# Performance work log

Hardware: AMD Instinct MI355X
Metric: run time of the kernel (lower is better)

Reference implementation:

```python
import jax, jax.numpy as jnp
import numpy as np

HIDDEN = 128
N_LAYERS = 6
N_NODES = 50000
N_EDGES = 640000


def _glorot(key, shape):
    fan_in, fan_out = shape[0], shape[1]
    lim = (6.0 / (fan_in + fan_out)) ** 0.5
    return jax.random.uniform(key, shape, jnp.float32, -lim, lim)


def setup_inputs() -> dict:
    key = jax.random.key(0)
    ks = jax.random.split(key, 8)
    pos = jax.random.normal(ks[0], (N_NODES, 3), jnp.float32)
    edge_attr = jax.random.normal(ks[1], (N_EDGES, 3), jnp.float32)
    edge_index = jax.random.randint(ks[2], (2, N_EDGES), 0, N_NODES, jnp.int64)
    enc_w = _glorot(ks[3], (3, HIDDEN)); enc_b = jnp.zeros((HIDDEN,), jnp.float32)
    dec_w = _glorot(ks[4], (HIDDEN, 3)); dec_b = jnp.zeros((3,), jnp.float32)
    lk = jax.random.split(ks[5], 4 * N_LAYERS)
    edge_w1 = jnp.stack([_glorot(lk[4 * i + 0], (3 * HIDDEN, HIDDEN)) for i in range(N_LAYERS)])
    edge_w2 = jnp.stack([_glorot(lk[4 * i + 1], (HIDDEN, HIDDEN)) for i in range(N_LAYERS)])
    node_w1 = jnp.stack([_glorot(lk[4 * i + 2], (2 * HIDDEN, HIDDEN)) for i in range(N_LAYERS)])
    node_w2 = jnp.stack([_glorot(lk[4 * i + 3], (HIDDEN, HIDDEN)) for i in range(N_LAYERS)])
    edge_b1 = jnp.zeros((N_LAYERS, HIDDEN), jnp.float32)
    edge_b2 = jnp.zeros((N_LAYERS, HIDDEN), jnp.float32)
    node_b1 = jnp.zeros((N_LAYERS, HIDDEN), jnp.float32)
    node_b2 = jnp.zeros((N_LAYERS, HIDDEN), jnp.float32)
    return dict(pos=pos, edge_attr=edge_attr, edge_index=edge_index,
                enc_w=enc_w, enc_b=enc_b, dec_w=dec_w, dec_b=dec_b,
                edge_w1=edge_w1, edge_b1=edge_b1, edge_w2=edge_w2, edge_b2=edge_b2,
                node_w1=node_w1, node_b1=node_b1, node_w2=node_w2, node_b2=node_b2)


def _interaction(x, ef, src, dst, ew1, eb1, ew2, eb2, nw1, nb1, nw2, nb2, n_nodes):
    # message: concat(x_i=x[dst], x_j=x[src], edge_feature) -> edge MLP
    m = jnp.concatenate([x[dst], x[src], ef], axis=-1)            # [E, 3H]
    m = jax.nn.relu(m @ ew1 + eb1) @ ew2 + eb2                     # [E, H]
    # scatter-mean by target node
    sums = jax.ops.segment_sum(m, dst, num_segments=n_nodes)      # [N, H]
    cnt = jax.ops.segment_sum(jnp.ones((m.shape[0],), m.dtype), dst, num_segments=n_nodes)
    aggr = sums / jnp.maximum(cnt, 1.0)[:, None]
    node = jnp.concatenate([x, aggr], axis=-1)                     # [N, 2H]
    node = jax.nn.relu(node @ nw1 + nb1) @ nw2 + nb2               # [N, H]
    return x + node, ef + m


def reference(pos, edge_attr, edge_index, enc_w, enc_b, dec_w, dec_b,
              edge_w1, edge_b1, edge_w2, edge_b2,
              node_w1, node_b1, node_w2, node_b2):
    n_nodes = pos.shape[0]
    src = edge_index[0]
    dst = edge_index[1]
    x = jnp.zeros((n_nodes, HIDDEN), jnp.float32)
    ef = edge_attr @ enc_w + enc_b
    for i in range(N_LAYERS):
        x, ef = _interaction(x, ef, src, dst,
                             edge_w1[i], edge_b1[i], edge_w2[i], edge_b2[i],
                             node_w1[i], node_b1[i], node_w2[i], node_b2[i], n_nodes)
    out = x @ dec_w + dec_b                                        # [N, 3]
    # F.normalize(dim=1, eps=1e-12)
    norm = jnp.linalg.norm(out, axis=1, keepdims=True)
    return out / jnp.maximum(norm, 1e-12)
```

## Files before the change

kernel.cpp:

```cpp
#include <hip/hip_runtime.h>
#include <cstdint>

#define HIDDEN  128
#define NLAYERS 6
#define NNODES  50000
#define NEDGES  640000

typedef short short8 __attribute__((ext_vector_type(8)));
typedef float f32x4  __attribute__((ext_vector_type(4)));

__device__ __forceinline__ float bf2f(unsigned short u) {
    return __uint_as_float(((unsigned int)u) << 16);
}
__device__ __forceinline__ unsigned short f2bf(float f) {
    unsigned int u = __float_as_uint(f);
    unsigned int r = u + 0x7FFFu + ((u >> 16) & 1u);
    return (unsigned short)(r >> 16);
}
__device__ __forceinline__ unsigned int pack2(float a, float b) {
    return (unsigned int)f2bf(a) | ((unsigned int)f2bf(b) << 16);
}
__device__ __forceinline__ void unpack8(uint4 v, float* f) {
    f[0] = bf2f((unsigned short)(v.x & 0xffff)); f[1] = bf2f((unsigned short)(v.x >> 16));
    f[2] = bf2f((unsigned short)(v.y & 0xffff)); f[3] = bf2f((unsigned short)(v.y >> 16));
    f[4] = bf2f((unsigned short)(v.z & 0xffff)); f[5] = bf2f((unsigned short)(v.z >> 16));
    f[6] = bf2f((unsigned short)(v.w & 0xffff)); f[7] = bf2f((unsigned short)(v.w >> 16));
}

__global__ void detect_kernel(const int* __restrict__ ei, int* __restrict__ flag)
{
    int lane = threadIdx.x;
    int v = ei[2 * lane + 1];
    unsigned long long b = __ballot(v != 0);
    if (lane == 0) *flag = (b != 0ULL) ? 1 : 0;
}

__global__ void normidx_kernel(const int* __restrict__ ei, const int* __restrict__ flag,
                               int* __restrict__ s32, int* __restrict__ d32)
{
    int e = blockIdx.x * blockDim.x + threadIdx.x;
    if (e >= NEDGES) return;
    int s, d;
    if (*flag) { s = ei[e]; d = ei[NEDGES + e]; }
    else       { s = ei[2 * e]; d = ei[2 * (NEDGES + e)]; }
    s32[e] = min(max(s, 0), NNODES - 1);
    d32[e] = min(max(d, 0), NNODES - 1);
}

__global__ void degree_kernel(const int* __restrict__ dst, int* __restrict__ deg)
{
    int e = blockIdx.x * blockDim.x + threadIdx.x;
    if (e < NEDGES) atomicAdd(&deg[dst[e]], 1);
}

#define SCAN_T 1024
__global__ void scan_kernel(const int* __restrict__ deg, int* __restrict__ off,
                            int* __restrict__ cursor)
{
    __shared__ int part[SCAN_T];
    const int t = threadIdx.x;
    const int CH = (NNODES + SCAN_T - 1) / SCAN_T;
    const int base = t * CH;
    int s = 0;
    for (int i = 0; i < CH; ++i) {
        int idx = base + i;
        if (idx < NNODES) s += deg[idx];
    }
    part[t] = s;
    __syncthreads();
    for (int d = 1; d < SCAN_T; d <<= 1) {
        int v = (t >= d) ? part[t - d] : 0;
        __syncthreads();
        part[t] += v;
        __syncthreads();
    }
    int run = (t == 0) ? 0 : part[t - 1];
    for (int i = 0; i < CH; ++i) {
        int idx = base + i;
        if (idx < NNODES) {
            off[idx] = run;
            cursor[idx] = run;
            run += deg[idx];
        }
    }
    if (t == SCAN_T - 1) off[NNODES] = run;
}

__global__ void scatter_kernel(const int* __restrict__ s32, const int* __restrict__ d32,
                               int* __restrict__ cursor,
                               int* __restrict__ sp, int* __restrict__ dp, int* __restrict__ ep)
{
    int e = blockIdx.x * blockDim.x + threadIdx.x;
    if (e >= NEDGES) return;
    int d = d32[e];
    int p = atomicAdd(&cursor[d], 1);
    sp[p] = s32[e];
    dp[p] = d;
    ep[p] = e;
}

__global__ void transpose_kernel(const float* __restrict__ W, unsigned short* __restrict__ WT,
                                 int K, int N, int L)
{
    long idx = (long)blockIdx.x * 256 + threadIdx.x;
    long tot = (long)L * K * N;
    if (idx >= tot) return;
    int kn = (int)(idx % ((long)K * N));
    int l  = (int)(idx / ((long)K * N));
    int k = kn / N;
    int n = kn % N;
    WT[(long)l * K * N + (long)n * K + k] = f2bf(W[idx]);
}

__global__ void encode_kernel(const float* __restrict__ ea,
                              const float* __restrict__ w,
                              const float* __restrict__ b,
                              const int* __restrict__ ep,
                              unsigned short* __restrict__ ef)
{
    int idx = blockIdx.x * blockDim.x + threadIdx.x;
    int p = idx >> 5;
    if (p >= NEDGES) return;
    int e = ep[p];
    int j = (idx & 31) << 2;
    float a0 = ea[e * 3 + 0], a1 = ea[e * 3 + 1], a2 = ea[e * 3 + 2];
    float4 w0 = *(const float4*)(w + 0 * HIDDEN + j);
    float4 w1 = *(const float4*)(w + 1 * HIDDEN + j);
    float4 w2 = *(const float4*)(w + 2 * HIDDEN + j);
    float4 bb = *(const float4*)(b + j);
    ushort4 o;
    o.x = f2bf(fmaf(a0, w0.x, fmaf(a1, w1.x, fmaf(a2, w2.x, bb.x))));
    o.y = f2bf(fmaf(a0, w0.y, fmaf(a1, w1.y, fmaf(a2, w2.y, bb.y))));
    o.z = f2bf(fmaf(a0, w0.z, fmaf(a1, w1.z, fmaf(a2, w2.z, bb.z))));
    o.w = f2bf(fmaf(a0, w0.w, fmaf(a1, w1.w, fmaf(a2, w2.w, bb.w))));
    *(ushort4*)(ef + (long)p * HIDDEN + j) = o;
}

__global__ __launch_bounds__(256, 3)
void edge_layer_mfma(const unsigned short* __restrict__ Xa,
                     const unsigned short* __restrict__ Xb,
                     unsigned short* __restrict__ ef,
                     float* __restrict__ sums,
                     const int* __restrict__ sp,
                     const int* __restrict__ dp,
                     const unsigned short* __restrict__ W1T,
                     const float* __restrict__ b1,
                     const unsigned short* __restrict__ W2T,
                     const float* __restrict__ b2)
{
    __shared__ __align__(16) unsigned char buf[45056];
    unsigned short* As = (unsigned short*)buf;
    unsigned short* Hs = (unsigned short*)buf;
    unsigned short* Bs = (unsigned short*)(buf + 34816);
    __shared__ int dv[128];
    __shared__ int sv[128];

    const int tid = threadIdx.x;
    const long eb = (long)blockIdx.x * 128;
    if (tid < 128) dv[tid]       = dp[eb + tid];
    else           sv[tid - 128] = sp[eb + tid - 128];

    const int lane = tid & 63;
    const int wv   = tid >> 6;
    const int mn   = lane & 15;
    const int q    = lane >> 4;
    const int rr   = tid >> 1;
    const int o    = (tid & 1) << 4;
    const int bn   = tid >> 1;
    const int bk   = (tid & 1) << 4;

    f32x4 acc[2][8];
#pragma unroll
    for (int h = 0; h < 2; ++h)
#pragma unroll
        for (int t = 0; t < 8; ++t) acc[h][t] = (f32x4)0.0f;

    short8 efold0[4], efold1[4];

    uint4 pa0, pa1, pw0, pw1;
    {
        const unsigned short* epp = ef + (eb + rr) * HIDDEN + o;
        pa0 = *(const uint4*)epp;
        pa1 = *(const uint4*)(epp + 8);
        const unsigned short* wp = W1T + (long)bn * 384 + 256 + bk;
        pw0 = *(const uint4*)wp;
        pw1 = *(const uint4*)(wp + 8);
    }

    for (int c = 0; c < 4; ++c) {
        *(uint4*)&As[rr * 40 + o]      = pa0;
        *(uint4*)&As[rr * 40 + o + 8]  = pa1;
        *(uint4*)&Bs[bn * 40 + bk]     = pw0;
        *(uint4*)&Bs[bn * 40 + bk + 8] = pw1;
        __syncthreads();

        if (c + 1 < 4) {
            const int cn = c + 1;
            const unsigned short* epp = ef + (eb + rr) * HIDDEN + (cn << 5) + o;
            pa0 = *(const uint4*)epp;
            pa1 = *(const uint4*)(epp + 8);
            const unsigned short* wp = W1T + (long)bn * 384 + 256 + (cn << 5) + bk;
            pw0 = *(const uint4*)wp;
            pw1 = *(const uint4*)(wp + 8);
        }

        short8 af0 = *(short8*)&As[(wv * 32 + mn) * 40 + (q << 3)];
        short8 af1 = *(short8*)&As[(wv * 32 + 16 + mn) * 40 + (q << 3)];
        efold0[c] = af0;
        efold1[c] = af1;
#pragma unroll
        for (int nt = 0; nt < 8; ++nt) {
            short8 bf = *(short8*)&Bs[(nt * 16 + mn) * 40 + (q << 3)];
            acc[0][nt] = __builtin_amdgcn_mfma_f32_16x16x32_bf16(af0, bf, acc[0][nt], 0, 0, 0);
            acc[1][nt] = __builtin_amdgcn_mfma_f32_16x16x32_bf16(af1, bf, acc[1][nt], 0, 0, 0);
        }
        __syncthreads();
    }

#pragma unroll
    for (int h = 0; h < 2; ++h)
#pragma unroll
        for (int nt = 0; nt < 8; ++nt)
#pragma unroll
            for (int r = 0; r < 4; ++r)
                Hs[(wv * 32 + h * 16 + q * 4 + r) * 136 + nt * 16 + mn] = f2bf(acc[h][nt][r]);

    {
        const int row  = wv * 32 + (lane >> 1);
        const int ch   = (lane & 1) << 6;
        const unsigned short* xap = Xa + (long)dv[row] * HIDDEN + ch;
        const unsigned short* xbp = Xb + (long)sv[row] * HIDDEN + ch;
        unsigned short* hp = &Hs[row * 136 + ch];
#pragma unroll
        for (int i = 0; i < 8; ++i) {
            uint4 va = *(const uint4*)(xap + (i << 3));
            uint4 vb = *(const uint4*)(xbp + (i << 3));
            uint4 vp = *(uint4*)(hp + (i << 3));
            float fa[8], fb[8], fp[8];
            unpack8(va, fa); unpack8(vb, fb); unpack8(vp, fp);
            const float* bp = b1 + ch + (i << 3);
            uint4 nw;
            float h0 = fmaxf(fp[0] + fa[0] + fb[0] + bp[0], 0.0f);
            float h1 = fmaxf(fp[1] + fa[1] + fb[1] + bp[1], 0.0f);
            float h2 = fmaxf(fp[2] + fa[2] + fb[2] + bp[2], 0.0f);
            float h3 = fmaxf(fp[3] + fa[3] + fb[3] + bp[3], 0.0f);
            float h4 = fmaxf(fp[4] + fa[4] + fb[4] + bp[4], 0.0f);
            float h5 = fmaxf(fp[5] + fa[5] + fb[5] + bp[5], 0.0f);
            float h6 = fmaxf(fp[6] + fa[6] + fb[6] + bp[6], 0.0f);
            float h7 = fmaxf(fp[7] + fa[7] + fb[7] + bp[7], 0.0f);
            nw.x = pack2(h0, h1); nw.y = pack2(h2, h3);
            nw.z = pack2(h4, h5); nw.w = pack2(h6, h7);
            *(uint4*)(hp + (i << 3)) = nw;
        }
    }

    f32x4 acc2[2][8];
#pragma unroll
    for (int h = 0; h < 2; ++h)
#pragma unroll
        for (int t = 0; t < 8; ++t) acc2[h][t] = (f32x4)0.0f;
    {
        const unsigned short* wp = W2T + (long)bn * 128 + bk;
        pw0 = *(const uint4*)wp;
        pw1 = *(const uint4*)(wp + 8);
    }
    for (int c = 0; c < 4; ++c) {
        *(uint4*)&Bs[bn * 40 + bk]     = pw0;
        *(uint4*)&Bs[bn * 40 + bk + 8] = pw1;
        __syncthreads();
        if (c + 1 < 4) {
            const unsigned short* wp = W2T + (long)bn * 128 + ((c + 1) << 5) + bk;
            pw0 = *(const uint4*)wp;
            pw1 = *(const uint4*)(wp + 8);
        }
        short8 af0 = *(short8*)&Hs[(wv * 32 + mn) * 136 + (c << 5) + (q << 3)];
        short8 af1 = *(short8*)&Hs[(wv * 32 + 16 + mn) * 136 + (c << 5) + (q << 3)];
#pragma unroll
        for (int nt = 0; nt < 8; ++nt) {
            short8 bf = *(short8*)&Bs[(nt * 16 + mn) * 40 + (q << 3)];
            acc2[0][nt] = __builtin_amdgcn_mfma_f32_16x16x32_bf16(af0, bf, acc2[0][nt], 0, 0, 0);
            acc2[1][nt] = __builtin_amdgcn_mfma_f32_16x16x32_bf16(af1, bf, acc2[1][nt], 0, 0, 0);
        }
        __syncthreads();
    }

#pragma unroll
    for (int h = 0; h < 2; ++h)
#pragma unroll
        for (int nt = 0; nt < 8; ++nt) {
            float b2v = b2[nt * 16 + mn];
#pragma unroll
            for (int r = 0; r < 4; ++r)
                Hs[(wv * 32 + h * 16 + q * 4 + r) * 136 + nt * 16 + mn] = f2bf(acc2[h][nt][r] + b2v);
        }

#pragma unroll
    for (int h = 0; h < 2; ++h) {
        const int row = wv * 32 + h * 16 + mn;
        unsigned short* ep_ = ef + (eb + row) * HIDDEN + (q << 3);
#pragma unroll
        for (int c = 0; c < 4; ++c) {
            uint4 mh = *(uint4*)&Hs[row * 136 + (c << 5) + (q << 3)];
            float m[8], e[8];
            unpack8(mh, m);
            short8 eo = h ? efold1[c] : efold0[c];
            uint4 eu = *(uint4*)&eo;
            unpack8(eu, e);
            uint4 nw;
            nw.x = pack2(e[0] + m[0], e[1] + m[1]);
            nw.y = pack2(e[2] + m[2], e[3] + m[3]);
            nw.z = pack2(e[4] + m[4], e[5] + m[5]);
            nw.w = pack2(e[6] + m[6], e[7] + m[7]);
            *(uint4*)(ep_ + (c << 5)) = nw;
        }
    }

    {
        const int cp = (tid & 63) << 1;
        const int qr = tid >> 6;
        float s0 = 0.0f, s1 = 0.0f;
        int cur = dv[qr * 32];
        for (int r = 0; r < 32; ++r) {
            const int row = qr * 32 + r;
            const int d = dv[row];
            if (d != cur) {
                atomicAdd(&sums[(long)cur * HIDDEN + cp], s0);
                atomicAdd(&sums[(long)cur * HIDDEN + cp + 1], s1);
                s0 = 0.0f; s1 = 0.0f;
                cur = d;
            }
            unsigned int u = *(unsigned int*)&Hs[row * 136 + cp];
            s0 += bf2f((unsigned short)(u & 0xffff));
            s1 += bf2f((unsigned short)(u >> 16));
        }
        atomicAdd(&sums[(long)cur * HIDDEN + cp], s0);
        atomicAdd(&sums[(long)cur * HIDDEN + cp + 1], s1);
    }
}

__global__ __launch_bounds__(256, 4)
void node_layer_mfma(float* __restrict__ x,
                     float* __restrict__ sums,
                     const int* __restrict__ deg,
                     const unsigned short* __restrict__ N1T,
                     const float* __restrict__ b1,
                     const unsigned short* __restrict__ N2T,
                     const float* __restrict__ b2,
                     const unsigned short* __restrict__ W1Tn,
                     unsigned short* __restrict__ Xa,
                     unsigned short* __restrict__ Xb)
{
    __shared__ __align__(16) unsigned short As[64 * 40];
    __shared__ __align__(16) unsigned short Bs[128 * 40];
    __shared__ __align__(16) unsigned short Hs[64 * 136];
    __shared__ float cInv[64];

    const int tid = threadIdx.x;
    const long n0 = (long)blockIdx.x * 64;
    if (tid < 64) {
        long n = n0 + tid;
        cInv[tid] = (n < NNODES) ? 1.0f / fmaxf((float)deg[n], 1.0f) : 0.0f;
    }

    const int lane = tid & 63;
    const int wv   = tid >> 6;
    const int mn   = lane & 15;
    const int q    = lane >> 4;
    const int srow = tid >> 2;
    const int sseg = tid & 3;
    const int bn   = tid >> 1;
    const int bk   = (tid & 1) << 4;

    long nr = n0 + srow;
    if (nr >= NNODES) nr = NNODES - 1;

    __syncthreads();

    f32x4 acc[8];
#pragma unroll
    for (int t = 0; t < 8; ++t) acc[t] = (f32x4)0.0f;

    float4 pa0, pa1;
    uint4 pb0, pb1;
    {
        const float* spx = x + nr * HIDDEN + (sseg << 3);
        pa0 = *(const float4*)spx;
        pa1 = *(const float4*)(spx + 4);
        const unsigned short* wp = N1T + (long)bn * 256 + bk;
        pb0 = *(const uint4*)wp;
        pb1 = *(const uint4*)(wp + 8);
    }
    float scCur = 1.0f;
    for (int c = 0; c < 8; ++c) {
        {
            uint4 w;
            w.x = pack2(pa0.x * scCur, pa0.y * scCur); w.y = pack2(pa0.z * scCur, pa0.w * scCur);
            w.z = pack2(pa1.x * scCur, pa1.y * scCur); w.w = pack2(pa1.z * scCur, pa1.w * scCur);
            *(uint4*)&As[srow * 40 + (sseg << 3)] = w;
        }
        *(uint4*)&Bs[bn * 40 + bk]     = pb0;
        *(uint4*)&Bs[bn * 40 + bk + 8] = pb1;
        __syncthreads();
        if (c + 1 < 8) {
            const int cn = c + 1;
            const float* base = (cn < 4) ? x : sums;
            scCur = (cn < 4) ? 1.0f : cInv[srow];
            const float* spx = base + nr * HIDDEN + ((cn & 3) << 5) + (sseg << 3);
            pa0 = *(const float4*)spx;
            pa1 = *(const float4*)(spx + 4);
            const unsigned short* wp = N1T + (long)bn * 256 + (cn << 5) + bk;
            pb0 = *(const uint4*)wp;
            pb1 = *(const uint4*)(wp + 8);
        }
        short8 af = *(short8*)&As[(wv * 16 + mn) * 40 + (q << 3)];
#pragma unroll
        for (int nt = 0; nt < 8; ++nt) {
            short8 bf = *(short8*)&Bs[(nt * 16 + mn) * 40 + (q << 3)];
            acc[nt] = __builtin_amdgcn_mfma_f32_16x16x32_bf16(af, bf, acc[nt], 0, 0, 0);
        }
        __syncthreads();
    }

    {
        long row = n0 + srow;
        if (row < NNODES) {
            float4 z = make_float4(0.f, 0.f, 0.f, 0.f);
            float* p = sums + row * HIDDEN + (sseg << 5);
#pragma unroll
            for (int i = 0; i < 8; ++i) ((float4*)p)[i] = z;
        }
    }

#pragma unroll
    for (int nt = 0; nt < 8; ++nt) {
        float b1v = b1[nt * 16 + mn];
#pragma unroll
        for (int r = 0; r < 4; ++r) {
            float hv = fmaxf(acc[nt][r] + b1v, 0.0f);
            Hs[(wv * 16 + q * 4 + r) * 136 + nt * 16 + mn] = f2bf(hv);
        }
    }

    f32x4 acc2[8];
#pragma unroll
    for (int t = 0; t < 8; ++t) acc2[t] = (f32x4)0.0f;
    {
        const unsigned short* wp = N2T + (long)bn * 128 + bk;
        pb0 = *(const uint4*)wp;
        pb1 = *(const uint4*)(wp + 8);
    }
    for (int c = 0; c < 4; ++c) {
        *(uint4*)&Bs[bn * 40 + bk]     = pb0;
        *(uint4*)&Bs[bn * 40 + bk + 8] = pb1;
        __syncthreads();
        if (c + 1 < 4) {
            const unsigned short* wp = N2T + (long)bn * 128 + ((c + 1) << 5) + bk;
            pb0 = *(const uint4*)wp;
            pb1 = *(const uint4*)(wp + 8);
        }
        short8 af = *(short8*)&Hs[(wv * 16 + mn) * 136 + (c << 5) + (q << 3)];
#pragma unroll
        for (int nt = 0; nt < 8; ++nt) {
            short8 bf = *(short8*)&Bs[(nt * 16 + mn) * 40 + (q << 3)];
            acc2[nt] = __builtin_amdgcn_mfma_f32_16x16x32_bf16(af, bf, acc2[nt], 0, 0, 0);
        }
        __syncthreads();
    }

#pragma unroll
    for (int nt = 0; nt < 8; ++nt) {
        float b2v = b2[nt * 16 + mn];
#pragma unroll
        for (int r = 0; r < 4; ++r) {
            long row = n0 + wv * 16 + q * 4 + r;
            float xn = 0.0f;
            if (row < NNODES) {
                float* p = x + row * HIDDEN + nt * 16 + mn;
                xn = *p + acc2[nt][r] + b2v;
                *p = xn;
            }
            Hs[(wv * 16 + q * 4 + r) * 136 + nt * 16 + mn] = f2bf(xn);
        }
    }

    if (W1Tn) {
#pragma unroll
        for (int half = 0; half < 2; ++half) {
            f32x4 accN[8];
#pragma unroll
            for (int t = 0; t < 8; ++t) accN[t] = (f32x4)0.0f;
            const int kbase = half << 7;
            {
                const unsigned short* wp = W1Tn + (long)bn * 384 + kbase + bk;
                pb0 = *(const uint4*)wp;
                pb1 = *(const uint4*)(wp + 8);
            }
            for (int c = 0; c < 4; ++c) {
                *(uint4*)&Bs[bn * 40 + bk]     = pb0;
                *(uint4*)&Bs[bn * 40 + bk + 8] = pb1;
                __syncthreads();
                if (c + 1 < 4) {
                    const unsigned short* wp = W1Tn + (long)bn * 384 + kbase + ((c + 1) << 5) + bk;
                    pb0 = *(const uint4*)wp;
                    pb1 = *(const uint4*)(wp + 8);
                }
                short8 af = *(short8*)&Hs[(wv * 16 + mn) * 136 + (c << 5) + (q << 3)];
#pragma unroll
                for (int nt = 0; nt < 8; ++nt) {
                    short8 bf = *(short8*)&Bs[(nt * 16 + mn) * 40 + (q << 3)];
                    accN[nt] = __builtin_amdgcn_mfma_f32_16x16x32_bf16(af, bf, accN[nt], 0, 0, 0);
                }
                __syncthreads();
            }
            unsigned short* Xout = half ? Xb : Xa;
#pragma unroll
            for (int nt = 0; nt < 8; ++nt) {
#pragma unroll
                for (int r = 0; r < 4; ++r) {
                    long row = n0 + wv * 16 + q * 4 + r;
                    if (row < NNODES) {
                        Xout[row * HIDDEN + nt * 16 + mn] = f2bf(accN[nt][r]);
                    }
                }
            }
        }
    }
}

__global__ void decode_kernel(const float* __restrict__ x,
                              const float* __restrict__ w,
                              const float* __restrict__ b,
                              float* __restrict__ out)
{
    int gid = blockIdx.x * blockDim.x + threadIdx.x;
    int node = gid >> 6;
    int lane = threadIdx.x & 63;
    if (node >= NNODES) return;
    float a0 = 0.f, a1 = 0.f, a2 = 0.f;
#pragma unroll
    for (int k = lane; k < HIDDEN; k += 64) {
        float xv = x[(long)node * HIDDEN + k];
        a0 = fmaf(xv, w[k * 3 + 0], a0);
        a1 = fmaf(xv, w[k * 3 + 1], a1);
        a2 = fmaf(xv, w[k * 3 + 2], a2);
    }
#pragma unroll
    for (int off = 32; off > 0; off >>= 1) {
        a0 += __shfl_down(a0, off);
        a1 += __shfl_down(a1, off);
        a2 += __shfl_down(a2, off);
    }
    if (lane == 0) {
        a0 += b[0]; a1 += b[1]; a2 += b[2];
        float nrm = sqrtf(a0 * a0 + a1 * a1 + a2 * a2);
        float inv = 1.0f / fmaxf(nrm, 1e-12f);
        out[(long)node * 3 + 0] = a0 * inv;
        out[(long)node * 3 + 1] = a1 * inv;
        out[(long)node * 3 + 2] = a2 * inv;
    }
}

extern "C" void kernel_launch(void* const* d_in, const int* in_sizes, int n_in,
                              void* d_out, int out_size, void* d_ws, size_t ws_size,
                              hipStream_t stream)
{
    const float* edge_attr = (const float*)d_in[1];
    const int*   ei        = (const int*)d_in[2];
    const float* enc_w     = (const float*)d_in[3];
    const float* enc_b     = (const float*)d_in[4];
    const float* dec_w     = (const float*)d_in[5];
    const float* dec_b     = (const float*)d_in[6];
    const float* edge_w1   = (const float*)d_in[7];
    const float* edge_b1   = (const float*)d_in[8];
    const float* edge_w2   = (const float*)d_in[9];
    const float* edge_b2   = (const float*)d_in[10];
    const float* node_w1   = (const float*)d_in[11];
    const float* node_b1   = (const float*)d_in[12];
    const float* node_w2   = (const float*)d_in[13];
    const float* node_b2   = (const float*)d_in[14];

    char* ws = (char*)d_ws;
    unsigned short* ef  = (unsigned short*)(ws);
    float* x      = (float*)(ws + 163840000L);
    float* sums   = (float*)(ws + 189440000L);
    int*   src32  = (int*)  (ws + 215040000L);
    int*   dst32  = (int*)  (ws + 217600000L);
    int*   sp     = (int*)  (ws + 220160000L);
    int*   dp     = (int*)  (ws + 222720000L);
    int*   eperm  = (int*)  (ws + 225280000L);
    int*   deg    = (int*)  (ws + 227840000L);
    int*   off    = (int*)  (ws + 228040704L);
    int*   cursor = (int*)  (ws + 228241408L);
    int*   flag   = (int*)  (ws + 228442112L);
    unsigned short* W1T = (unsigned short*)(ws + 228442176L);
    unsigned short* W2T = (unsigned short*)(ws + 229032000L);
    unsigned short* N1T = (unsigned short*)(ws + 229228608L);
    unsigned short* N2T = (unsigned short*)(ws + 229621824L);
    unsigned short* Xa  = (unsigned short*)(ws + 229818432L);
    unsigned short* Xb  = (unsigned short*)(ws + 242618432L);

    float* out = (float*)d_out;

    hipMemsetAsync(x, 0, (size_t)NNODES * HIDDEN * sizeof(float), stream);
    hipMemsetAsync(sums, 0, (size_t)NNODES * HIDDEN * sizeof(float), stream);
    hipMemsetAsync(deg, 0, 200704, stream);
    hipMemsetAsync(Xa, 0, 25600000, stream);

    detect_kernel<<<1, 64, 0, stream>>>(ei, flag);
    normidx_kernel<<<(NEDGES + 255) / 256, 256, 0, stream>>>(ei, flag, src32, dst32);
    degree_kernel<<<(NEDGES + 255) / 256, 256, 0, stream>>>(dst32, deg);
    scan_kernel<<<1, SCAN_T, 0, stream>>>(deg, off, cursor);
    scatter_kernel<<<(NEDGES + 255) / 256, 256, 0, stream>>>(src32, dst32, cursor, sp, dp, eperm);
    encode_kernel<<<(NEDGES * 32 + 255) / 256, 256, 0, stream>>>(edge_attr, enc_w, enc_b, eperm, ef);

    transpose_kernel<<<(6 * 384 * 128 + 255) / 256, 256, 0, stream>>>(edge_w1, W1T, 384, 128, 6);
    transpose_kernel<<<(6 * 128 * 128 + 255) / 256, 256, 0, stream>>>(edge_w2, W2T, 128, 128, 6);
    transpose_kernel<<<(6 * 256 * 128 + 255) / 256, 256, 0, stream>>>(node_w1, N1T, 256, 128, 6);
    transpose_kernel<<<(6 * 128 * 128 + 255) / 256, 256, 0, stream>>>(node_w2, N2T, 128, 128, 6);

    for (int l = 0; l < NLAYERS; ++l) {
        edge_layer_mfma<<<NEDGES / 128, 256, 0, stream>>>(
            Xa, Xb, ef, sums, sp, dp,
            W1T + (long)l * 384 * 128, edge_b1 + (long)l * HIDDEN,
            W2T + (long)l * 128 * 128, edge_b2 + (long)l * HIDDEN);
        const unsigned short* w1next = (l + 1 < NLAYERS) ? (W1T + (long)(l + 1) * 384 * 128) : nullptr;
        node_layer_mfma<<<(NNODES + 63) / 64, 256, 0, stream>>>(
            x, sums, deg,
            N1T + (long)l * 256 * 128, node_b1 + (long)l * HIDDEN,
            N2T + (long)l * 128 * 128, node_b2 + (long)l * HIDDEN,
            w1next, Xa, Xb);
    }

    decode_kernel<<<(NNODES * 64 + 255) / 256, 256, 0, stream>>>(x, dec_w, dec_b, out);
}
```

Before: 1.544 ms.

## Pre-swizzle node MLP weights into MFMA fragment order and drop LDS staging

Adds a swizzle kernel that reorders node and next-layer edge weights into the per-lane MFMA B-fragment layout, so the node kernel reads B operands straight from global/L2 instead of staging them through shared memory with barriers. The node kernel now uses 32-row, 128-thread blocks, loads the whole x/aggr row into LDS once, and zeroes sums up front. This removes many __syncthreads and LDS round trips, at the cost of every wave re-reading weights from cache and smaller blocks.

```diff
diff --git a/kernel.cpp b/kernel.cpp
--- a/kernel.cpp
+++ b/kernel.cpp
@@ -110,6 +110,23 @@
     int k = kn / N;
     int n = kn % N;
     WT[(long)l * K * N + (long)n * K + k] = f2bf(W[idx]);
+}
+
+__global__ void swizzle_kernel(const float* __restrict__ W, unsigned short* __restrict__ out,
+                               int k0, int Ktot, int Ksw, int L)
+{
+    long per = (long)Ksw * 128;
+    long idx = (long)blockIdx.x * 256 + threadIdx.x;
+    if (idx >= (long)L * per) return;
+    int l = (int)(idx / per);
+    int o = (int)(idx % per);
+    int j    = o & 7;
+    int lane = (o >> 3) & 63;
+    int frag = o >> 9;
+    int c = frag >> 3, nt = frag & 7;
+    int k = k0 + c * 32 + (lane >> 4) * 8 + j;
+    int n = nt * 16 + (lane & 15);
+    out[idx] = f2bf(W[(long)l * Ktot * 128 + (long)k * 128 + n]);
 }
 
 __global__ void encode_kernel(const float* __restrict__ ea,
@@ -338,96 +355,68 @@
     }
 }
 
-__global__ __launch_bounds__(256, 4)
+__global__ __launch_bounds__(128, 4)
 void node_layer_mfma(float* __restrict__ x,
                      float* __restrict__ sums,
                      const int* __restrict__ deg,
-                     const unsigned short* __restrict__ N1T,
+                     const unsigned short* __restrict__ N1S,
                      const float* __restrict__ b1,
-                     const unsigned short* __restrict__ N2T,
+                     const unsigned short* __restrict__ N2S,
                      const float* __restrict__ b2,
-                     const unsigned short* __restrict__ W1Tn,
+                     const unsigned short* __restrict__ W1An,
+                     const unsigned short* __restrict__ W1Bn,
                      unsigned short* __restrict__ Xa,
                      unsigned short* __restrict__ Xb)
 {
-    __shared__ __align__(16) unsigned short As[64 * 40];
-    __shared__ __align__(16) unsigned short Bs[128 * 40];
-    __shared__ __align__(16) unsigned short Hs[64 * 136];
-    __shared__ float cInv[64];
-
-    const int tid = threadIdx.x;
-    const long n0 = (long)blockIdx.x * 64;
-    if (tid < 64) {
-        long n = n0 + tid;
-        cInv[tid] = (n < NNODES) ? 1.0f / fmaxf((float)deg[n], 1.0f) : 0.0f;
-    }
-
+    __shared__ __align__(16) unsigned short As[32 * 264];
+    __shared__ __align__(16) unsigned short Hs[32 * 136];
+
+    const int tid  = threadIdx.x;
+    const long n0  = (long)blockIdx.x * 32;
     const int lane = tid & 63;
     const int wv   = tid >> 6;
     const int mn   = lane & 15;
     const int q    = lane >> 4;
-    const int srow = tid >> 2;
-    const int sseg = tid & 3;
-    const int bn   = tid >> 1;
-    const int bk   = (tid & 1) << 4;
-
-    long nr = n0 + srow;
-    if (nr >= NNODES) nr = NNODES - 1;
-
-    __syncthreads();
+
+    {
+        const int row = tid >> 2;
+        const int qt  = (tid & 3) << 5;
+        long nr = n0 + row; if (nr >= NNODES) nr = NNODES - 1;
+        const float ci = 1.0f / fmaxf((float)deg[nr], 1.0f);
+        const float* xr = x + nr * HIDDEN + qt;
+        const float* sr = sums + nr * HIDDEN + qt;
+#pragma unroll
+        for (int i = 0; i < 4; ++i) {
+            float4 v0 = *(const float4*)(xr + i * 8);
+            float4 v1 = *(const float4*)(xr + i * 8 + 4);
+            uint4 u;
+            u.x = pack2(v0.x, v0.y); u.y = pack2(v0.z, v0.w);
+            u.z = pack2(v1.x, v1.y); u.w = pack2(v1.z, v1.w);
+            *(uint4*)&As[row * 264 + qt + i * 8] = u;
+            float4 w0 = *(const float4*)(sr + i * 8);
+            float4 w1 = *(const float4*)(sr + i * 8 + 4);
+            u.x = pack2(w0.x * ci, w0.y * ci); u.y = pack2(w0.z * ci, w0.w * ci);
+            u.z = pack2(w1.x * ci, w1.y * ci); u.w = pack2(w1.z * ci, w1.w * ci);
+            *(uint4*)&As[row * 264 + 128 + qt + i * 8] = u;
+        }
+        if (n0 + row < NNODES) {
+            float4 z = make_float4(0.f, 0.f, 0.f, 0.f);
+            float* p = sums + nr * HIDDEN + qt;
+#pragma unroll
+            for (int i = 0; i < 8; ++i) ((float4*)p)[i] = z;
+        }
+    }
 
     f32x4 acc[8];
 #pragma unroll
     for (int t = 0; t < 8; ++t) acc[t] = (f32x4)0.0f;
-
-    float4 pa0, pa1;
-    uint4 pb0, pb1;
-    {
-        const float* spx = x + nr * HIDDEN + (sseg << 3);
-        pa0 = *(const float4*)spx;
-        pa1 = *(const float4*)(spx + 4);
-        const unsigned short* wp = N1T + (long)bn * 256 + bk;
-        pb0 = *(const uint4*)wp;
-        pb1 = *(const uint4*)(wp + 8);
-    }
-    float scCur = 1.0f;
+#pragma unroll
     for (int c = 0; c < 8; ++c) {
-        {
-            uint4 w;
-            w.x = pack2(pa0.x * scCur, pa0.y * scCur); w.y = pack2(pa0.z * scCur, pa0.w * scCur);
-            w.z = pack2(pa1.x * scCur, pa1.y * scCur); w.w = pack2(pa1.z * scCur, pa1.w * scCur);
-            *(uint4*)&As[srow * 40 + (sseg << 3)] = w;
-        }
-        *(uint4*)&Bs[bn * 40 + bk]     = pb0;
-        *(uint4*)&Bs[bn * 40 + bk + 8] = pb1;
-        __syncthreads();
-        if (c + 1 < 8) {
-            const int cn = c + 1;
-            const float* base = (cn < 4) ? x : sums;
-            scCur = (cn < 4) ? 1.0f : cInv[srow];
-            const float* spx = base + nr * HIDDEN + ((cn & 3) << 5) + (sseg << 3);
-            pa0 = *(const float4*)spx;
-            pa1 = *(const float4*)(spx + 4);
-            const unsigned short* wp = N1T + (long)bn * 256 + (cn << 5) + bk;
-            pb0 = *(const uint4*)wp;
-            pb1 = *(const uint4*)(wp + 8);
-        }
-        short8 af = *(short8*)&As[(wv * 16 + mn) * 40 + (q << 3)];
+        short8 af = *(short8*)&As[(wv * 16 + mn) * 264 + (c << 5) + (q << 3)];
 #pragma unroll
         for (int nt = 0; nt < 8; ++nt) {
-            short8 bf = *(short8*)&Bs[(nt * 16 + mn) * 40 + (q << 3)];
+            short8 bf = *(const short8*)(N1S + (c * 8 + nt) * 512 + lane * 8);
             acc[nt] = __builtin_amdgcn_mfma_f32_16x16x32_bf16(af, bf, acc[nt], 0, 0, 0);
-        }
-        __syncthreads();
-    }
-
-    {
-        long row = n0 + srow;
-        if (row < NNODES) {
-            float4 z = make_float4(0.f, 0.f, 0.f, 0.f);
-            float* p = sums + row * HIDDEN + (sseg << 5);
-#pragma unroll
-            for (int i = 0; i < 8; ++i) ((float4*)p)[i] = z;
         }
     }
 
@@ -444,27 +433,14 @@
     f32x4 acc2[8];
 #pragma unroll
     for (int t = 0; t < 8; ++t) acc2[t] = (f32x4)0.0f;
-    {
-        const unsigned short* wp = N2T + (long)bn * 128 + bk;
-        pb0 = *(const uint4*)wp;
-        pb1 = *(const uint4*)(wp + 8);
-    }
+#pragma unroll
     for (int c = 0; c < 4; ++c) {
-        *(uint4*)&Bs[bn * 40 + bk]     = pb0;
-        *(uint4*)&Bs[bn * 40 + bk + 8] = pb1;
-        __syncthreads();
-        if (c + 1 < 4) {
-            const unsigned short* wp = N2T + (long)bn * 128 + ((c + 1) << 5) + bk;
-            pb0 = *(const uint4*)wp;
-            pb1 = *(const uint4*)(wp + 8);
-        }
         short8 af = *(short8*)&Hs[(wv * 16 + mn) * 136 + (c << 5) + (q << 3)];
 #pragma unroll
         for (int nt = 0; nt < 8; ++nt) {
-            short8 bf = *(short8*)&Bs[(nt * 16 + mn) * 40 + (q << 3)];
+            short8 bf = *(const short8*)(N2S + (c * 8 + nt) * 512 + lane * 8);
             acc2[nt] = __builtin_amdgcn_mfma_f32_16x16x32_bf16(af, bf, acc2[nt], 0, 0, 0);
         }
-        __syncthreads();
     }
 
 #pragma unroll
@@ -483,34 +459,21 @@
         }
     }
 
-    if (W1Tn) {
+    if (W1An) {
 #pragma unroll
         for (int half = 0; half < 2; ++half) {
+            const unsigned short* Bsw = half ? W1Bn : W1An;
             f32x4 accN[8];
 #pragma unroll
             for (int t = 0; t < 8; ++t) accN[t] = (f32x4)0.0f;
-            const int kbase = half << 7;
-            {
-                const unsigned short* wp = W1Tn + (long)bn * 384 + kbase + bk;
-                pb0 = *(const uint4*)wp;
-                pb1 = *(const uint4*)(wp + 8);
-            }
+#pragma unroll
             for (int c = 0; c < 4; ++c) {
-                *(uint4*)&Bs[bn * 40 + bk]     = pb0;
-                *(uint4*)&Bs[bn * 40 + bk + 8] = pb1;
-                __syncthreads();
-                if (c + 1 < 4) {
-                    const unsigned short* wp = W1Tn + (long)bn * 384 + kbase + ((c + 1) << 5) + bk;
-                    pb0 = *(const uint4*)wp;
-                    pb1 = *(const uint4*)(wp + 8);
-                }
                 short8 af = *(short8*)&Hs[(wv * 16 + mn) * 136 + (c << 5) + (q << 3)];
 #pragma unroll
                 for (int nt = 0; nt < 8; ++nt) {
-                    short8 bf = *(short8*)&Bs[(nt * 16 + mn) * 40 + (q << 3)];
+                    short8 bf = *(const short8*)(Bsw + (c * 8 + nt) * 512 + lane * 8);
                     accN[nt] = __builtin_amdgcn_mfma_f32_16x16x32_bf16(af, bf, accN[nt], 0, 0, 0);
                 }
-                __syncthreads();
             }
             unsigned short* Xout = half ? Xb : Xa;
 #pragma unroll
@@ -594,10 +557,12 @@
     int*   flag   = (int*)  (ws + 228442112L);
     unsigned short* W1T = (unsigned short*)(ws + 228442176L);
     unsigned short* W2T = (unsigned short*)(ws + 229032000L);
-    unsigned short* N1T = (unsigned short*)(ws + 229228608L);
-    unsigned short* N2T = (unsigned short*)(ws + 229621824L);
-    unsigned short* Xa  = (unsigned short*)(ws + 229818432L);
-    unsigned short* Xb  = (unsigned short*)(ws + 242618432L);
+    unsigned short* N1S = (unsigned short*)(ws + 229228608L);
+    unsigned short* N2S = (unsigned short*)(ws + 229621824L);
+    unsigned short* W1A = (unsigned short*)(ws + 229818432L);
+    unsigned short* W1B = (unsigned short*)(ws + 230015040L);
+    unsigned short* Xa  = (unsigned short*)(ws + 230211648L);
+    unsigned short* Xb  = (unsigned short*)(ws + 243011648L);
 
     float* out = (float*)d_out;
 
@@ -615,20 +580,23 @@
 
     transpose_kernel<<<(6 * 384 * 128 + 255) / 256, 256, 0, stream>>>(edge_w1, W1T, 384, 128, 6);
     transpose_kernel<<<(6 * 128 * 128 + 255) / 256, 256, 0, stream>>>(edge_w2, W2T, 128, 128, 6);
-    transpose_kernel<<<(6 * 256 * 128 + 255) / 256, 256, 0, stream>>>(node_w1, N1T, 256, 128, 6);
-    transpose_kernel<<<(6 * 128 * 128 + 255) / 256, 256, 0, stream>>>(node_w2, N2T, 128, 128, 6);
+    swizzle_kernel<<<(6 * 256 * 128 + 255) / 256, 256, 0, stream>>>(node_w1, N1S, 0,   256, 256, 6);
+    swizzle_kernel<<<(6 * 128 * 128 + 255) / 256, 256, 0, stream>>>(node_w2, N2S, 0,   128, 128, 6);
+    swizzle_kernel<<<(6 * 128 * 128 + 255) / 256, 256, 0, stream>>>(edge_w1, W1A, 0,   384, 128, 6);
+    swizzle_kernel<<<(6 * 128 * 128 + 255) / 256, 256, 0, stream>>>(edge_w1, W1B, 128, 384, 128, 6);
 
     for (int l = 0; l < NLAYERS; ++l) {
         edge_layer_mfma<<<NEDGES / 128, 256, 0, stream>>>(
             Xa, Xb, ef, sums, sp, dp,
             W1T + (long)l * 384 * 128, edge_b1 + (long)l * HIDDEN,
             W2T + (long)l * 128 * 128, edge_b2 + (long)l * HIDDEN);
-        const unsigned short* w1next = (l + 1 < NLAYERS) ? (W1T + (long)(l + 1) * 384 * 128) : nullptr;
-        node_layer_mfma<<<(NNODES + 63) / 64, 256, 0, stream>>>(
+        const unsigned short* w1an = (l + 1 < NLAYERS) ? (W1A + (long)(l + 1) * 16384) : nullptr;
+        const unsigned short* w1bn = (l + 1 < NLAYERS) ? (W1B + (long)(l + 1) * 16384) : nullptr;
+        node_layer_mfma<<<(NNODES + 31) / 32, 128, 0, stream>>>(
             x, sums, deg,
-            N1T + (long)l * 256 * 128, node_b1 + (long)l * HIDDEN,
-            N2T + (long)l * 128 * 128, node_b2 + (long)l * HIDDEN,
-            w1next, Xa, Xb);
+            N1S + (long)l * 32768, node_b1 + (long)l * HIDDEN,
+            N2S + (long)l * 16384, node_b2 + (long)l * HIDDEN,
+            w1an, w1bn, Xa, Xb);
     }
 
     decode_kernel<<<(NNODES * 64 + 255) / 256, 256, 0, stream>>>(x, dec_w, dec_b, out);
```

New measurement: 1.680 ms. +8.7%, slower.

## Split edge-layer work across 8 waves and alias node-layer shared buffers

Applied to the files above, without the earlier changes.

The edge MLP kernel now runs 512 threads per 128-edge block, so each wave handles 16 rows instead of 32. This halves the accumulator and saved-ef registers per thread and allows more waves in flight to hide gather and atomic latency. The node kernel overlays its A staging buffer with the H buffer in shared memory to lower LDS use and raises its occupancy hint. The cost is that each B fragment read from LDS now feeds half as many MFMAs, and the block barriers cover more waves.

```diff
diff --git a/kernel.cpp b/kernel.cpp
--- a/kernel.cpp
+++ b/kernel.cpp
@@ -136,7 +136,7 @@
     *(ushort4*)(ef + (long)p * HIDDEN + j) = o;
 }
 
-__global__ __launch_bounds__(256, 3)
+__global__ __launch_bounds__(512, 6)
 void edge_layer_mfma(const unsigned short* __restrict__ Xa,
                      const unsigned short* __restrict__ Xb,
                      unsigned short* __restrict__ ef,
@@ -157,82 +157,65 @@
 
     const int tid = threadIdx.x;
     const long eb = (long)blockIdx.x * 128;
-    if (tid < 128) dv[tid]       = dp[eb + tid];
-    else           sv[tid - 128] = sp[eb + tid - 128];
+    if (tid < 128)       dv[tid]       = dp[eb + tid];
+    else if (tid < 256)  sv[tid - 128] = sp[eb + tid - 128];
 
     const int lane = tid & 63;
     const int wv   = tid >> 6;
     const int mn   = lane & 15;
     const int q    = lane >> 4;
-    const int rr   = tid >> 1;
-    const int o    = (tid & 1) << 4;
-    const int bn   = tid >> 1;
-    const int bk   = (tid & 1) << 4;
-
-    f32x4 acc[2][8];
-#pragma unroll
-    for (int h = 0; h < 2; ++h)
-#pragma unroll
-        for (int t = 0; t < 8; ++t) acc[h][t] = (f32x4)0.0f;
-
-    short8 efold0[4], efold1[4];
-
-    uint4 pa0, pa1, pw0, pw1;
-    {
-        const unsigned short* epp = ef + (eb + rr) * HIDDEN + o;
-        pa0 = *(const uint4*)epp;
-        pa1 = *(const uint4*)(epp + 8);
-        const unsigned short* wp = W1T + (long)bn * 384 + 256 + bk;
-        pw0 = *(const uint4*)wp;
-        pw1 = *(const uint4*)(wp + 8);
+    const int rr   = tid >> 2;
+    const int o    = (tid & 3) << 3;
+    const int bn   = tid >> 2;
+    const int bo   = (tid & 3) << 3;
+
+    f32x4 acc[8];
+#pragma unroll
+    for (int t = 0; t < 8; ++t) acc[t] = (f32x4)0.0f;
+
+    short8 efold[4];
+
+    uint4 pa, pw;
+    {
+        pa = *(const uint4*)(ef + (eb + rr) * HIDDEN + o);
+        pw = *(const uint4*)(W1T + (long)bn * 384 + 256 + bo);
     }
 
     for (int c = 0; c < 4; ++c) {
-        *(uint4*)&As[rr * 40 + o]      = pa0;
-        *(uint4*)&As[rr * 40 + o + 8]  = pa1;
-        *(uint4*)&Bs[bn * 40 + bk]     = pw0;
-        *(uint4*)&Bs[bn * 40 + bk + 8] = pw1;
+        *(uint4*)&As[rr * 40 + o]  = pa;
+        *(uint4*)&Bs[bn * 40 + bo] = pw;
         __syncthreads();
 
         if (c + 1 < 4) {
             const int cn = c + 1;
-            const unsigned short* epp = ef + (eb + rr) * HIDDEN + (cn << 5) + o;
-            pa0 = *(const uint4*)epp;
-            pa1 = *(const uint4*)(epp + 8);
-            const unsigned short* wp = W1T + (long)bn * 384 + 256 + (cn << 5) + bk;
-            pw0 = *(const uint4*)wp;
-            pw1 = *(const uint4*)(wp + 8);
-        }
-
-        short8 af0 = *(short8*)&As[(wv * 32 + mn) * 40 + (q << 3)];
-        short8 af1 = *(short8*)&As[(wv * 32 + 16 + mn) * 40 + (q << 3)];
-        efold0[c] = af0;
-        efold1[c] = af1;
+            pa = *(const uint4*)(ef + (eb + rr) * HIDDEN + (cn << 5) + o);
+            pw = *(const uint4*)(W1T + (long)bn * 384 + 256 + (cn << 5) + bo);
+        }
+
+        short8 af = *(short8*)&As[(wv * 16 + mn) * 40 + (q << 3)];
+        efold[c] = af;
 #pragma unroll
         for (int nt = 0; nt < 8; ++nt) {
             short8 bf = *(short8*)&Bs[(nt * 16 + mn) * 40 + (q << 3)];
-            acc[0][nt] = __builtin_amdgcn_mfma_f32_16x16x32_bf16(af0, bf, acc[0][nt], 0, 0, 0);
-            acc[1][nt] = __builtin_amdgcn_mfma_f32_16x16x32_bf16(af1, bf, acc[1][nt], 0, 0, 0);
-        }
-        __syncthreads();
-    }
-
-#pragma unroll
-    for (int h = 0; h < 2; ++h)
-#pragma unroll
-        for (int nt = 0; nt < 8; ++nt)
-#pragma unroll
-            for (int r = 0; r < 4; ++r)
-                Hs[(wv * 32 + h * 16 + q * 4 + r) * 136 + nt * 16 + mn] = f2bf(acc[h][nt][r]);
-
-    {
-        const int row  = wv * 32 + (lane >> 1);
-        const int ch   = (lane & 1) << 6;
+            acc[nt] = __builtin_amdgcn_mfma_f32_16x16x32_bf16(af, bf, acc[nt], 0, 0, 0);
+        }
+        __syncthreads();
+    }
+
+#pragma unroll
+    for (int nt = 0; nt < 8; ++nt)
+#pragma unroll
+        for (int r = 0; r < 4; ++r)
+            Hs[(wv * 16 + q * 4 + r) * 136 + nt * 16 + mn] = f2bf(acc[nt][r]);
+
+    {
+        const int row = wv * 16 + (lane >> 2);
+        const int ch  = (lane & 3) << 5;
         const unsigned short* xap = Xa + (long)dv[row] * HIDDEN + ch;
         const unsigned short* xbp = Xb + (long)sv[row] * HIDDEN + ch;
         unsigned short* hp = &Hs[row * 136 + ch];
 #pragma unroll
-        for (int i = 0; i < 8; ++i) {
+        for (int i = 0; i < 4; ++i) {
             uint4 va = *(const uint4*)(xap + (i << 3));
             uint4 vb = *(const uint4*)(xbp + (i << 3));
             uint4 vp = *(uint4*)(hp + (i << 3));
@@ -254,57 +237,44 @@
         }
     }
 
-    f32x4 acc2[2][8];
-#pragma unroll
-    for (int h = 0; h < 2; ++h)
-#pragma unroll
-        for (int t = 0; t < 8; ++t) acc2[h][t] = (f32x4)0.0f;
-    {
-        const unsigned short* wp = W2T + (long)bn * 128 + bk;
-        pw0 = *(const uint4*)wp;
-        pw1 = *(const uint4*)(wp + 8);
+    f32x4 acc2[8];
+#pragma unroll
+    for (int t = 0; t < 8; ++t) acc2[t] = (f32x4)0.0f;
+    {
+        pw = *(const uint4*)(W2T + (long)bn * 128 + bo);
     }
     for (int c = 0; c < 4; ++c) {
-        *(uint4*)&Bs[bn * 40 + bk]     = pw0;
-        *(uint4*)&Bs[bn * 40 + bk + 8] = pw1;
+        *(uint4*)&Bs[bn * 40 + bo] = pw;
         __syncthreads();
         if (c + 1 < 4) {
-            const unsigned short* wp = W2T + (long)bn * 128 + ((c + 1) << 5) + bk;
-            pw0 = *(const uint4*)wp;
-            pw1 = *(const uint4*)(wp + 8);
-        }
-        short8 af0 = *(short8*)&Hs[(wv * 32 + mn) * 136 + (c << 5) + (q << 3)];
-        short8 af1 = *(short8*)&Hs[(wv * 32 + 16 + mn) * 136 + (c << 5) + (q << 3)];
+            pw = *(const uint4*)(W2T + (long)bn * 128 + ((c + 1) << 5) + bo);
+        }
+        short8 af = *(short8*)&Hs[(wv * 16 + mn) * 136 + (c << 5) + (q << 3)];
 #pragma unroll
         for (int nt = 0; nt < 8; ++nt) {
             short8 bf = *(short8*)&Bs[(nt * 16 + mn) * 40 + (q << 3)];
-            acc2[0][nt] = __builtin_amdgcn_mfma_f32_16x16x32_bf16(af0, bf, acc2[0][nt], 0, 0, 0);
-            acc2[1][nt] = __builtin_amdgcn_mfma_f32_16x16x32_bf16(af1, bf, acc2[1][nt], 0, 0, 0);
-        }
-        __syncthreads();
-    }
-
-#pragma unroll
-    for (int h = 0; h < 2; ++h)
-#pragma unroll
-        for (int nt = 0; nt < 8; ++nt) {
-            float b2v = b2[nt * 16 + mn];
-#pragma unroll
-            for (int r = 0; r < 4; ++r)
-                Hs[(wv * 32 + h * 16 + q * 4 + r) * 136 + nt * 16 + mn] = f2bf(acc2[h][nt][r] + b2v);
-        }
-
-#pragma unroll
-    for (int h = 0; h < 2; ++h) {
-        const int row = wv * 32 + h * 16 + mn;
+            acc2[nt] = __builtin_amdgcn_mfma_f32_16x16x32_bf16(af, bf, acc2[nt], 0, 0, 0);
+        }
+        __syncthreads();
+    }
+
+#pragma unroll
+    for (int nt = 0; nt < 8; ++nt) {
+        float b2v = b2[nt * 16 + mn];
+#pragma unroll
+        for (int r = 0; r < 4; ++r)
+            Hs[(wv * 16 + q * 4 + r) * 136 + nt * 16 + mn] = f2bf(acc2[nt][r] + b2v);
+    }
+
+    {
+        const int row = wv * 16 + mn;
         unsigned short* ep_ = ef + (eb + row) * HIDDEN + (q << 3);
 #pragma unroll
         for (int c = 0; c < 4; ++c) {
             uint4 mh = *(uint4*)&Hs[row * 136 + (c << 5) + (q << 3)];
             float m[8], e[8];
             unpack8(mh, m);
-            short8 eo = h ? efold1[c] : efold0[c];
-            uint4 eu = *(uint4*)&eo;
+            uint4 eu = *(uint4*)&efold[c];
             unpack8(eu, e);
             uint4 nw;
             nw.x = pack2(e[0] + m[0], e[1] + m[1]);
@@ -316,12 +286,11 @@
     }
 
     {
-        const int cp = (tid & 63) << 1;
-        const int qr = tid >> 6;
+        const int cp = lane << 1;
         float s0 = 0.0f, s1 = 0.0f;
-        int cur = dv[qr * 32];
-        for (int r = 0; r < 32; ++r) {
-            const int row = qr * 32 + r;
+        int cur = dv[wv * 16];
+        for (int r = 0; r < 16; ++r) {
+            const int row = wv * 16 + r;
             const int d = dv[row];
             if (d != cur) {
                 atomicAdd(&sums[(long)cur * HIDDEN + cp], s0);
@@ -338,7 +307,7 @@
     }
 }
 
-__global__ __launch_bounds__(256, 4)
+__global__ __launch_bounds__(256, 5)
 void node_layer_mfma(float* __restrict__ x,
                      float* __restrict__ sums,
                      const int* __restrict__ deg,
@@ -350,9 +319,10 @@
                      unsigned short* __restrict__ Xa,
                      unsigned short* __restrict__ Xb)
 {
-    __shared__ __align__(16) unsigned short As[64 * 40];
-    __shared__ __align__(16) unsigned short Bs[128 * 40];
-    __shared__ __align__(16) unsigned short Hs[64 * 136];
+    __shared__ __align__(16) unsigned char nbuf[27648];
+    unsigned short* As = (unsigned short*)nbuf;
+    unsigned short* Hs = (unsigned short*)nbuf;
+    unsigned short* Bs = (unsigned short*)(nbuf + 17408);
     __shared__ float cInv[64];
 
     const int tid = threadIdx.x;
@@ -619,7 +589,7 @@
     transpose_kernel<<<(6 * 128 * 128 + 255) / 256, 256, 0, stream>>>(node_w2, N2T, 128, 128, 6);
 
     for (int l = 0; l < NLAYERS; ++l) {
-        edge_layer_mfma<<<NEDGES / 128, 256, 0, stream>>>(
+        edge_layer_mfma<<<NEDGES / 128, 512, 0, stream>>>(
             Xa, Xb, ef, sums, sp, dp,
             W1T + (long)l * 384 * 128, edge_b1 + (long)l * HIDDEN,
             W2T + (long)l * 128 * 128, edge_b2 + (long)l * HIDDEN);
```

After: 1.554 ms. No clear change (+0.6%).
